# Kernel tuning notes

Hardware: AMD Instinct MI355X
Metric: run time of the kernel (lower is better)

Reference implementation:

```python
import jax, jax.numpy as jnp
import numpy as np

N = 50000          # nodes
E = 800000         # edges (before self-loops)
F_IN = 256         # feature_dim
HEADS = 3
OUT = 128          # per-head channels
HO = HEADS * OUT   # 384
NUM_GRAPHS = 64
NUM_CLASSES = 2
SLOPE = 0.2        # PyG GATConv default negative_slope


def setup_inputs() -> dict:
    key = jax.random.key(0)
    ks = jax.random.split(key, 8)
    x = jax.random.normal(ks[0], (N, F_IN), dtype=jnp.float32)
    edge_index = jax.random.randint(ks[1], (2, E), 0, N)
    batch = jnp.sort(jax.random.randint(ks[2], (N,), 0, NUM_GRAPHS))
    # GATConv params (glorot-ish scales)
    W = jax.random.normal(ks[3], (F_IN, HO), dtype=jnp.float32) * (1.0 / np.sqrt(F_IN))
    att_src = jax.random.normal(ks[4], (HEADS, OUT), dtype=jnp.float32) * 0.1
    att_dst = jax.random.normal(ks[5], (HEADS, OUT), dtype=jnp.float32) * 0.1
    bias = jnp.zeros((HO,), dtype=jnp.float32)
    fc_w = jax.random.normal(ks[6], (HO, NUM_CLASSES), dtype=jnp.float32) * 0.05
    fc_b = jnp.zeros((NUM_CLASSES,), dtype=jnp.float32)
    return {"x": x, "edge_index": edge_index, "batch": batch, "W": W,
            "att_src": att_src, "att_dst": att_dst, "bias": bias,
            "fc_w": fc_w, "fc_b": fc_b}


def reference(x, edge_index, batch, W, att_src, att_dst, bias, fc_w, fc_b):
    n = x.shape[0]
    h = (x @ W).reshape(n, HEADS, OUT)                      # [N, H, C]
    # add self-loops (PyG default add_self_loops=True)
    loops = jnp.arange(n)
    src = jnp.concatenate([edge_index[0], loops])           # [E+N]
    dst = jnp.concatenate([edge_index[1], loops])
    # per-node attention logits
    a_src = jnp.einsum('nhc,hc->nh', h, att_src)            # [N, H]
    a_dst = jnp.einsum('nhc,hc->nh', h, att_dst)
    e = jax.nn.leaky_relu(a_src[src] + a_dst[dst], SLOPE)   # [E+N, H]
    # segment softmax over incoming edges of each dst node
    emax = jax.ops.segment_max(e, dst, num_segments=n)
    ex = jnp.exp(e - emax[dst])
    denom = jax.ops.segment_sum(ex, dst, num_segments=n)
    alpha = ex / (denom[dst] + 1e-16)                       # [E+N, H]
    # weighted scatter-add aggregation
    msg = h[src] * alpha[:, :, None]                        # [E+N, H, C]
    out = jax.ops.segment_sum(msg, dst, num_segments=n)     # [N, H, C]
    out = jax.nn.relu(out.reshape(n, HO) + bias)            # [N, 384]
    # global mean pool per graph
    counts = jax.ops.segment_sum(jnp.ones((n,), out.dtype), batch,
                                 num_segments=NUM_GRAPHS)
    pooled = jax.ops.segment_sum(out, batch, num_segments=NUM_GRAPHS)
    pooled = pooled / jnp.maximum(counts, 1.0)[:, None]     # [G, 384]
    return pooled @ fc_w + fc_b                             # [G, num_classes]
```

## Files before the change

kernel.cpp:

```cpp
#include <hip/hip_runtime.h>
#include <hip/hip_bf16.h>
#include <math.h>

#define HEADS 3
#define HO 384
#define NGRAPH 64
#define F_IN 256
#define SLOPE 0.2f

typedef __attribute__((ext_vector_type(8))) short bf8;
typedef __attribute__((ext_vector_type(4))) float f4;
typedef __attribute__((ext_vector_type(2))) unsigned u2v;
typedef __attribute__((ext_vector_type(4))) unsigned u4v;

__device__ __forceinline__ unsigned short bfr(float f) {
    unsigned u = __float_as_uint(f);
    u += 0x7fffu + ((u >> 16) & 1u);
    return (unsigned short)(u >> 16);
}
__device__ __forceinline__ float bflo(unsigned u) { return __uint_as_float(u << 16); }
__device__ __forceinline__ float bfhi(unsigned u) { return __uint_as_float(u & 0xffff0000u); }
__device__ __forceinline__ float lrelu(float v) { return (v > 0.f) ? v : SLOPE * v; }

__device__ __forceinline__ void mix2(float& a0, float& a1, unsigned h2, float wm) {
    asm("v_fma_mix_f32 %0, %2, %3, %0 op_sel:[0,0,0] op_sel_hi:[1,0,0]\n\t"
        "v_fma_mix_f32 %1, %2, %3, %1 op_sel:[1,0,0] op_sel_hi:[1,0,0]"
        : "+v"(a0), "+v"(a1)
        : "v"(h2), "v"(wm));
}
__device__ __forceinline__ void dec8_mix(float* acc, float wm, unsigned ux, unsigned uy,
                                         unsigned c64) {
    unsigned p0 = __builtin_amdgcn_perm(ux, c64, 0x00050004u);
    unsigned p1 = __builtin_amdgcn_perm(ux, c64, 0x00070006u);
    unsigned p2 = __builtin_amdgcn_perm(uy, c64, 0x00050004u);
    unsigned p3 = __builtin_amdgcn_perm(uy, c64, 0x00070006u);
    mix2(acc[0], acc[1], p0, wm);
    mix2(acc[2], acc[3], p1, wm);
    mix2(acc[4], acc[5], p2, wm);
    mix2(acc[6], acc[7], p3, wm);
}

__global__ __launch_bounds__(256) void misc_k(const int* __restrict__ ei,
                                              const float* __restrict__ W,
                                              const int* __restrict__ batch,
                                              const float* __restrict__ X,
                                              int* __restrict__ count,
                                              int* __restrict__ rank,
                                              short* __restrict__ WbT,
                                              short* __restrict__ Xb,
                                              int* __restrict__ gstart,
                                              int NBc, int E, int N) {
    int b = blockIdx.x;
    if (b < NBc) {
        int e = b * 256 + threadIdx.x;
        int ET = E + N;
        if (e >= ET) return;
        int d = (e < E) ? ei[E + e] : (e - E);
        rank[e] = atomicAdd(&count[d], 1);
    } else if (b < NBc + 384) {
        int n = b - NBc;
        int k = threadIdx.x;
        WbT[n * 256 + k] = (short)bfr(W[(size_t)k * HO + n]);
    } else if (b == NBc + 384) {
        int g = threadIdx.x;
        if (g > NGRAPH) return;
        int lo = 0, hi = N;
        while (lo < hi) { int mid = (lo + hi) >> 1; if (batch[mid] < g) lo = mid + 1; else hi = mid; }
        gstart[g] = lo;
    } else {
        size_t base = (size_t)(b - (NBc + 385)) * 2048 + threadIdx.x * 8;
        if (base + 8 <= (size_t)N * F_IN) {
            float4 q0 = *(const float4*)(X + base);
            float4 q1 = *(const float4*)(X + base + 4);
            bf8 pk;
            pk[0] = (short)bfr(q0.x); pk[1] = (short)bfr(q0.y);
            pk[2] = (short)bfr(q0.z); pk[3] = (short)bfr(q0.w);
            pk[4] = (short)bfr(q1.x); pk[5] = (short)bfr(q1.y);
            pk[6] = (short)bfr(q1.z); pk[7] = (short)bfr(q1.w);
            *(bf8*)(Xb + base) = pk;
        }
    }
}

__global__ __launch_bounds__(256, 2) void gemm_att(const short* __restrict__ Xb,
                                                   const short* __restrict__ WbT,
                                                   const float* __restrict__ att_src,
                                                   const float* __restrict__ att_dst,
                                                   unsigned char* __restrict__ hc,
                                                   float* __restrict__ ni,
                                                   float* __restrict__ aDstO, int N) {
    __shared__ float lsS[64][8];
    __shared__ float lsD[64][8];
    __shared__ float lsM[64][8];
    __shared__ float sclS[64][4];
    int t = threadIdx.x;
    int w = t >> 6, lane = t & 63;
    int quad = lane >> 4, l15 = lane & 15;
    int rbase = blockIdx.x * 64;

    f4 acc[4][6] = {};
    const short* ap[4];
#pragma unroll
    for (int at = 0; at < 4; at++) {
        int r = rbase + at * 16 + l15;
        r = (r < N) ? r : (N - 1);
        ap[at] = Xb + (size_t)r * F_IN + quad * 8;
    }
    const short* bp = WbT + (size_t)(w * 96 + l15) * F_IN + quad * 8;

#pragma unroll
    for (int k0 = 0; k0 < F_IN; k0 += 32) {
        bf8 ar[4], br[6];
#pragma unroll
        for (int at = 0; at < 4; at++)
            ar[at] = *(const bf8*)(ap[at] + k0);
#pragma unroll
        for (int nt = 0; nt < 6; nt++)
            br[nt] = *(const bf8*)(bp + nt * 16 * F_IN + k0);
#pragma unroll
        for (int at = 0; at < 4; at++)
#pragma unroll
            for (int nt = 0; nt < 6; nt++)
                acc[at][nt] = __builtin_amdgcn_mfma_f32_16x16x32_bf16(ar[at], br[nt], acc[at][nt], 0, 0, 0);
    }

    const int splits[4] = {6, 2, 4, 0};
    int split = splits[w];
    float asv[6], adv[6];
#pragma unroll
    for (int nt = 0; nt < 6; nt++) {
        int c = w * 96 + nt * 16 + l15;
        asv[nt] = att_src[c];
        adv[nt] = att_dst[c];
    }
#pragma unroll
    for (int at = 0; at < 4; at++) {
#pragma unroll
        for (int r = 0; r < 4; r++) {
            float paS = 0.f, pbS = 0.f, paD = 0.f, pbD = 0.f;
#pragma unroll
            for (int nt = 0; nt < 6; nt++) {
                float v = acc[at][nt][r];
                if (nt < split) { paS += v * asv[nt]; paD += v * adv[nt]; }
                else            { pbS += v * asv[nt]; pbD += v * adv[nt]; }
            }
#pragma unroll
            for (int off = 1; off < 16; off <<= 1) {
                paS += __shfl_xor(paS, off); pbS += __shfl_xor(pbS, off);
                paD += __shfl_xor(paD, off); pbD += __shfl_xor(pbD, off);
            }
            if (l15 == 0) {
                int row = at * 16 + quad * 4 + r;
                lsS[row][w * 2 + 0] = paS; lsS[row][w * 2 + 1] = pbS;
                lsD[row][w * 2 + 0] = paD; lsD[row][w * 2 + 1] = pbD;
            }
        }
    }
#pragma unroll
    for (int at = 0; at < 4; at++) {
#pragma unroll
        for (int r = 0; r < 4; r++) {
            float pa = 0.f, pb = 0.f;
#pragma unroll
            for (int nt = 0; nt < 6; nt++) {
                float v = fabsf(acc[at][nt][r]);
                if (nt < split) pa = fmaxf(pa, v); else pb = fmaxf(pb, v);
            }
#pragma unroll
            for (int off = 1; off < 16; off <<= 1) {
                pa = fmaxf(pa, __shfl_xor(pa, off));
                pb = fmaxf(pb, __shfl_xor(pb, off));
            }
            if (l15 == 0) {
                int row = at * 16 + quad * 4 + r;
                lsM[row][w * 2 + 0] = pa; lsM[row][w * 2 + 1] = pb;
            }
        }
    }
    __syncthreads();
    if (t < 64) {
        float s0 = fmaxf(lsM[t][0], lsM[t][2]);
        float s1 = fmaxf(lsM[t][3], lsM[t][4]);
        float s2 = fmaxf(lsM[t][5], lsM[t][7]);
        sclS[t][0] = (s0 > 0.f) ? 127.f / s0 : 0.f;
        sclS[t][1] = (s1 > 0.f) ? 127.f / s1 : 0.f;
        sclS[t][2] = (s2 > 0.f) ? 127.f / s2 : 0.f;
        int node = rbase + t;
        if (node < N) {
            aDstO[node * 3 + 0] = lsD[t][0] + lsD[t][2];
            aDstO[node * 3 + 1] = lsD[t][3] + lsD[t][4];
            aDstO[node * 3 + 2] = lsD[t][5] + lsD[t][7];
            float4 nA, nB;
            nA.x = lsS[t][0] + lsS[t][2];
            nA.y = lsS[t][3] + lsS[t][4];
            nA.z = lsS[t][5] + lsS[t][7];
            nA.w = s0 / 127.f;
            nB.x = s1 / 127.f;
            nB.y = s2 / 127.f;
            nB.z = 0.f; nB.w = 0.f;
            *(float4*)(ni + (size_t)node * 8) = nA;
            *(float4*)(ni + (size_t)node * 8 + 4) = nB;
        }
    }
    __syncthreads();
#pragma unroll
    for (int at = 0; at < 4; at++) {
#pragma unroll
        for (int nt = 0; nt < 6; nt++) {
            int hd = (w * 96 + nt * 16) >> 7;
#pragma unroll
            for (int r = 0; r < 4; r++) {
                int row = at * 16 + quad * 4 + r;
                int node = rbase + row;
                float rq = sclS[row][hd];
                int qi = (int)rintf(acc[at][nt][r] * rq) + 128;
                if (node < N) hc[(size_t)node * 384 + w * 96 + nt * 16 + l15] = (unsigned char)qi;
            }
        }
    }
}

__global__ __launch_bounds__(256) void scan_a(const int* __restrict__ count,
                                              int* __restrict__ offsets,
                                              int* __restrict__ bsums, int N) {
    __shared__ int tmp[256];
    int t = threadIdx.x;
    int i = blockIdx.x * 256 + t;
    int v = (i < N) ? count[i] : 0;
    tmp[t] = v;
    __syncthreads();
    for (int off = 1; off < 256; off <<= 1) {
        int x = (t >= off) ? tmp[t - off] : 0;
        __syncthreads();
        tmp[t] += x;
        __syncthreads();
    }
    if (i < N) offsets[i] = tmp[t] - v;
    if (t == 255) bsums[blockIdx.x] = tmp[255];
}

__global__ __launch_bounds__(256) void scan_b(int* __restrict__ bsums, int NB) {
    __shared__ int tmp[256];
    int t = threadIdx.x;
    int v = (t < NB) ? bsums[t] : 0;
    tmp[t] = v;
    __syncthreads();
    for (int off = 1; off < 256; off <<= 1) {
        int x = (t >= off) ? tmp[t - off] : 0;
        __syncthreads();
        tmp[t] += x;
        __syncthreads();
    }
    if (t < NB) bsums[t] = tmp[t] - v;
}

__global__ __launch_bounds__(256) void scan_c(int* __restrict__ offsets,
                                              const int* __restrict__ bsums, int N) {
    int i = blockIdx.x * 256 + threadIdx.x;
    if (i < N) offsets[i] += bsums[blockIdx.x];
}

__global__ __launch_bounds__(256) void scatter_k(const int* __restrict__ ei,
                                                 const int* __restrict__ rank,
                                                 const int* __restrict__ offsets,
                                                 int* __restrict__ csr_src, int E, int N) {
    int e = blockIdx.x * 256 + threadIdx.x;
    int ET = E + N;
    if (e >= ET) return;
    int s, d;
    if (e < E) { s = ei[e]; d = ei[E + e]; } else { s = e - E; d = s; }
    csr_src[offsets[d] + rank[e]] = s;
}

__global__ __launch_bounds__(256) void aggregate_k(const unsigned* __restrict__ hcw,
                                                   const int* __restrict__ csr_src,
                                                   const int* __restrict__ offsets,
                                                   const int* __restrict__ count,
                                                   const float* __restrict__ ni,
                                                   const float* __restrict__ a_dst,
                                                   const float* __restrict__ bias,
                                                   unsigned* __restrict__ outb, int N) {
    __shared__ float ws[4][3][68];
    __shared__ int   si[4][64];
    int wv = threadIdx.x >> 6;
    int wid = blockIdx.x * 4 + wv;
    int lane = threadIdx.x & 63;
    if (wid >= N) return;
    int start = offsets[wid], n = count[wid];
    float ad0 = a_dst[wid * 3 + 0], ad1 = a_dst[wid * 3 + 1], ad2 = a_dst[wid * 3 + 2];
    int hm = (lane < 48) ? (lane >> 4) : 0;
    int off = (lane < 48) ? 2 * lane : 0;
    float acc[8] = {0.f, 0.f, 0.f, 0.f, 0.f, 0.f, 0.f, 0.f};
    float wsum = 0.f;
    float i0, i1, i2;
    const unsigned c64 = 0x64646464u;

    if (n <= 64) {
        int sreg = 0;
        float l0 = -INFINITY, l1 = -INFINITY, l2 = -INFINITY;
        float s0v = 0.f, s1v = 0.f, s2v = 0.f;
        if (lane < n) {
            sreg = csr_src[start + lane];
            float4 A = *(const float4*)(ni + (size_t)sreg * 8);
            float4 B = *(const float4*)(ni + (size_t)sreg * 8 + 4);
            l0 = lrelu(A.x + ad0); l1 = lrelu(A.y + ad1); l2 = lrelu(A.z + ad2);
            s0v = A.w; s1v = B.x; s2v = B.y;
        }
        float m0 = l0, m1 = l1, m2 = l2;
#pragma unroll
        for (int o = 1; o < 64; o <<= 1) {
            m0 = fmaxf(m0, __shfl_xor(m0, o));
            m1 = fmaxf(m1, __shfl_xor(m1, o));
            m2 = fmaxf(m2, __shfl_xor(m2, o));
        }
        float e0 = (lane < n) ? expf(l0 - m0) : 0.f;
        float e1 = (lane < n) ? expf(l1 - m1) : 0.f;
        float e2 = (lane < n) ? expf(l2 - m2) : 0.f;
        float s0 = e0, s1 = e1, s2 = e2;
#pragma unroll
        for (int o = 1; o < 64; o <<= 1) {
            s0 += __shfl_xor(s0, o);
            s1 += __shfl_xor(s1, o);
            s2 += __shfl_xor(s2, o);
        }
        i0 = 1.f / (s0 + 1e-16f); i1 = 1.f / (s1 + 1e-16f); i2 = 1.f / (s2 + 1e-16f);
        ws[wv][0][lane] = e0 * s0v;
        ws[wv][1][lane] = e1 * s1v;
        ws[wv][2][lane] = e2 * s2v;
        si[wv][lane] = sreg;
        __builtin_amdgcn_wave_barrier();

        for (int j = 0; j < n; j += 8) {
            int4 ia = *(const int4*)&si[wv][j];
            int4 ib = *(const int4*)&si[wv][j + 4];
            u2v u0 = *(const u2v*)(hcw + (size_t)ia.x * 96 + off);
            u2v u1 = *(const u2v*)(hcw + (size_t)ia.y * 96 + off);
            u2v u2 = *(const u2v*)(hcw + (size_t)ia.z * 96 + off);
            u2v u3 = *(const u2v*)(hcw + (size_t)ia.w * 96 + off);
            u2v u4 = *(const u2v*)(hcw + (size_t)ib.x * 96 + off);
            u2v u5 = *(const u2v*)(hcw + (size_t)ib.y * 96 + off);
            u2v u6 = *(const u2v*)(hcw + (size_t)ib.z * 96 + off);
            u2v u7 = *(const u2v*)(hcw + (size_t)ib.w * 96 + off);
            float4 wa = *(const float4*)&ws[wv][hm][j];
            float4 wb = *(const float4*)&ws[wv][hm][j + 4];
            wsum += (wa.x + wa.y + wa.z + wa.w) + (wb.x + wb.y + wb.z + wb.w);
            dec8_mix(acc, wa.x, u0.x, u0.y, c64);
            dec8_mix(acc, wa.y, u1.x, u1.y, c64);
            dec8_mix(acc, wa.z, u2.x, u2.y, c64);
            dec8_mix(acc, wa.w, u3.x, u3.y, c64);
            dec8_mix(acc, wb.x, u4.x, u4.y, c64);
            dec8_mix(acc, wb.y, u5.x, u5.y, c64);
            dec8_mix(acc, wb.z, u6.x, u6.y, c64);
            dec8_mix(acc, wb.w, u7.x, u7.y, c64);
        }
    } else {
        float m0 = -INFINITY, m1 = -INFINITY, m2 = -INFINITY;
        for (int j = lane; j < n; j += 64) {
            int s = csr_src[start + j];
            float4 A = *(const float4*)(ni + (size_t)s * 8);
            m0 = fmaxf(m0, lrelu(A.x + ad0));
            m1 = fmaxf(m1, lrelu(A.y + ad1));
            m2 = fmaxf(m2, lrelu(A.z + ad2));
        }
#pragma unroll
        for (int o = 1; o < 64; o <<= 1) {
            m0 = fmaxf(m0, __shfl_xor(m0, o));
            m1 = fmaxf(m1, __shfl_xor(m1, o));
            m2 = fmaxf(m2, __shfl_xor(m2, o));
        }
        float s0 = 0.f, s1 = 0.f, s2 = 0.f;
        for (int j = lane; j < n; j += 64) {
            int s = csr_src[start + j];
            float4 A = *(const float4*)(ni + (size_t)s * 8);
            s0 += expf(lrelu(A.x + ad0) - m0);
            s1 += expf(lrelu(A.y + ad1) - m1);
            s2 += expf(lrelu(A.z + ad2) - m2);
        }
#pragma unroll
        for (int o = 1; o < 64; o <<= 1) {
            s0 += __shfl_xor(s0, o);
            s1 += __shfl_xor(s1, o);
            s2 += __shfl_xor(s2, o);
        }
        i0 = 1.f / (s0 + 1e-16f); i1 = 1.f / (s1 + 1e-16f); i2 = 1.f / (s2 + 1e-16f);
        for (int j = 0; j < n; j++) {
            int s = csr_src[start + j];
            float4 A = *(const float4*)(ni + (size_t)s * 8);
            float4 B = *(const float4*)(ni + (size_t)s * 8 + 4);
            float w0 = expf(lrelu(A.x + ad0) - m0) * A.w;
            float w1 = expf(lrelu(A.y + ad1) - m1) * B.x;
            float w2 = expf(lrelu(A.z + ad2) - m2) * B.y;
            float wm = (hm == 0) ? w0 : ((hm == 1) ? w1 : w2);
            u2v u = *(const u2v*)(hcw + (size_t)s * 96 + off);
            wsum += wm;
            dec8_mix(acc, wm, u.x, u.y, c64);
        }
    }

    if (lane < 48) {
        float im = (hm == 0) ? i0 : ((hm == 1) ? i1 : i2);
        float corr = 1152.f * wsum;
        float4 b0 = *(const float4*)(bias + 8 * lane);
        float4 b1 = *(const float4*)(bias + 8 * lane + 4);
        float bb[8] = {b0.x, b0.y, b0.z, b0.w, b1.x, b1.y, b1.z, b1.w};
        u4v pk;
#pragma unroll
        for (int j = 0; j < 4; j++) {
            float x0 = (acc[2 * j] - corr) * im + bb[2 * j];
            float x1 = (acc[2 * j + 1] - corr) * im + bb[2 * j + 1];
            x0 = (x0 > 0.f) ? x0 : 0.f;
            x1 = (x1 > 0.f) ? x1 : 0.f;
            pk[j] = (unsigned)bfr(x0) | ((unsigned)bfr(x1) << 16);
        }
        *(u4v*)(outb + (size_t)wid * 192 + 4 * lane) = pk;
    }
}

__global__ __launch_bounds__(192) void pool_k(const unsigned* __restrict__ outb,
                                              const int* __restrict__ gstart,
                                              float* __restrict__ pooled) {
    int g = blockIdx.x;
    int chunk = blockIdx.y;
    int t = threadIdx.x;
    int lo = gstart[g], hi = gstart[g + 1];
    float al = 0.f, ah = 0.f;
    for (int r = lo + chunk; r < hi; r += 8) {
        unsigned u = outb[(size_t)r * 192 + t];
        al += bflo(u);
        ah += bfhi(u);
    }
    atomicAdd(&pooled[g * HO + 2 * t], al);
    atomicAdd(&pooled[g * HO + 2 * t + 1], ah);
}

__global__ __launch_bounds__(64) void fc_k(const float* __restrict__ pooled,
                                           const int* __restrict__ gstart,
                                           const float* __restrict__ fc_w,
                                           const float* __restrict__ fc_b,
                                           float* __restrict__ out) {
    int g = blockIdx.x;
    int lane = threadIdx.x;
    float a0 = 0.f, a1 = 0.f;
#pragma unroll
    for (int k = 0; k < 6; k++) {
        int c = lane + 64 * k;
        float pv = pooled[g * HO + c];
        a0 += pv * fc_w[c * 2 + 0];
        a1 += pv * fc_w[c * 2 + 1];
    }
#pragma unroll
    for (int off = 32; off > 0; off >>= 1) {
        a0 += __shfl_down(a0, off);
        a1 += __shfl_down(a1, off);
    }
    if (lane == 0) {
        float cnt = fmaxf((float)(gstart[g + 1] - gstart[g]), 1.0f);
        out[g * 2 + 0] = a0 / cnt + fc_b[0];
        out[g * 2 + 1] = a1 / cnt + fc_b[1];
    }
}

extern "C" void kernel_launch(void* const* d_in, const int* in_sizes, int n_in,
                              void* d_out, int out_size, void* d_ws, size_t ws_size,
                              hipStream_t stream) {
    const float* x       = (const float*)d_in[0];
    const int*   ei      = (const int*)d_in[1];
    const int*   batch   = (const int*)d_in[2];
    const float* W       = (const float*)d_in[3];
    const float* att_src = (const float*)d_in[4];
    const float* att_dst = (const float*)d_in[5];
    const float* bias    = (const float*)d_in[6];
    const float* fc_w    = (const float*)d_in[7];
    const float* fc_b    = (const float*)d_in[8];
    float* out = (float*)d_out;

    const int N = in_sizes[2];
    const int E = in_sizes[1] / 2;
    const int ET = E + N;

    char* p = (char*)d_ws;
    auto alloc = [&](size_t bytes) -> char* {
        char* r = p;
        p += (bytes + 255) & ~(size_t)255;
        return r;
    };
    short*         wbt    = (short*)alloc((size_t)HO * F_IN * 2);
    short*         xb     = (short*)alloc((size_t)N * F_IN * 2);
    unsigned char* hc     = (unsigned char*)alloc((size_t)N * 384);
    unsigned*      outb   = (unsigned*)alloc((size_t)N * 192 * 4);
    float*         ni     = (float*)alloc((size_t)N * 8 * 4);
    float*         a_dst  = (float*)alloc((size_t)N * 3 * 4);
    char*          zstart = p;
    int*           count  = (int*)alloc((size_t)N * 4);
    float*         pooled = (float*)alloc((size_t)NGRAPH * HO * 4);
    size_t         zbytes = (size_t)(p - zstart);
    int*           offsets = (int*)alloc((size_t)N * 4);
    int*           rank    = (int*)alloc((size_t)ET * 4);
    int*           bsums   = (int*)alloc(4096);
    int*           gstart  = (int*)alloc(1024);
    int*           csr_src = (int*)alloc((size_t)ET * 4);

    hipMemsetAsync(zstart, 0, zbytes, stream);

    int NBc = (ET + 255) / 256;
    int NXc = (int)(((size_t)N * F_IN + 2047) / 2048);
    misc_k<<<NBc + 384 + 1 + NXc, 256, 0, stream>>>(ei, W, batch, x, count, rank,
                                                    wbt, xb, gstart, NBc, E, N);
    gemm_att<<<(N + 63) / 64, 256, 0, stream>>>(xb, wbt, att_src, att_dst,
                                                hc, ni, a_dst, N);
    int NB = (N + 255) / 256;
    scan_a<<<NB, 256, 0, stream>>>(count, offsets, bsums, N);
    scan_b<<<1, 256, 0, stream>>>(bsums, NB);
    scan_c<<<NB, 256, 0, stream>>>(offsets, bsums, N);
    scatter_k<<<(ET + 255) / 256, 256, 0, stream>>>(ei, rank, offsets, csr_src, E, N);
    aggregate_k<<<(N + 3) / 4, 256, 0, stream>>>((const unsigned*)hc, csr_src, offsets,
                                                 count, ni, a_dst, bias, outb, N);
    dim3 pg(NGRAPH, 8);
    pool_k<<<pg, 192, 0, stream>>>(outb, gstart, pooled);
    fc_k<<<NGRAPH, 64, 0, stream>>>(pooled, gstart, fc_w, fc_b, out);

    (void)n_in; (void)out_size; (void)ws_size;
}
```

Baseline: 309.1 us.

## Fold attention vectors into weight matrix and compute logits via extra MFMA

Precomputes W·att_src and W·att_dst per head as a small bf16 matrix, so the attention logits come from an extra MFMA tile on one wave. This replaces the per-row dot products and shuffle reductions over the projected features in the epilogue. The GEMM tile is also halved to 32 rows with higher occupancy (launch bounds 4). Logits now come from the bf16-rounded folded weights rather than the fp32 accumulators, which slightly changes precision. The fourth wave also does extra MFMA work, adding imbalance across waves.

Result: no change. 308.3 us (-0.2%).

```diff
diff --git a/kernel.cpp b/kernel.cpp
--- a/kernel.cpp
+++ b/kernel.cpp
@@ -44,9 +44,12 @@
                                               const float* __restrict__ W,
                                               const int* __restrict__ batch,
                                               const float* __restrict__ X,
+                                              const float* __restrict__ att_src,
+                                              const float* __restrict__ att_dst,
                                               int* __restrict__ count,
                                               int* __restrict__ rank,
                                               short* __restrict__ WbT,
+                                              short* __restrict__ WaT,
                                               short* __restrict__ Xb,
                                               int* __restrict__ gstart,
                                               int NBc, int E, int N) {
@@ -67,8 +70,23 @@
         int lo = 0, hi = N;
         while (lo < hi) { int mid = (lo + hi) >> 1; if (batch[mid] < g) lo = mid + 1; else hi = mid; }
         gstart[g] = lo;
+    } else if (b == NBc + 385) {
+        int k = threadIdx.x;
+        float s[6] = {0.f, 0.f, 0.f, 0.f, 0.f, 0.f};
+        const float* wr = W + (size_t)k * HO;
+        for (int h = 0; h < 3; h++) {
+            float a0 = 0.f, a1 = 0.f;
+            for (int c = 0; c < 128; c++) {
+                float wv = wr[h * 128 + c];
+                a0 += wv * att_src[h * 128 + c];
+                a1 += wv * att_dst[h * 128 + c];
+            }
+            s[h] = a0; s[3 + h] = a1;
+        }
+        for (int c = 0; c < 6; c++)  WaT[c * 256 + k] = (short)bfr(s[c]);
+        for (int c = 6; c < 16; c++) WaT[c * 256 + k] = 0;
     } else {
-        size_t base = (size_t)(b - (NBc + 385)) * 2048 + threadIdx.x * 8;
+        size_t base = (size_t)(b - (NBc + 386)) * 2048 + threadIdx.x * 8;
         if (base + 8 <= (size_t)N * F_IN) {
             float4 q0 = *(const float4*)(X + base);
             float4 q1 = *(const float4*)(X + base + 4);
@@ -82,82 +100,57 @@
     }
 }
 
-__global__ __launch_bounds__(256, 2) void gemm_att(const short* __restrict__ Xb,
+__global__ __launch_bounds__(256, 4) void gemm_att(const short* __restrict__ Xb,
                                                    const short* __restrict__ WbT,
-                                                   const float* __restrict__ att_src,
-                                                   const float* __restrict__ att_dst,
+                                                   const short* __restrict__ WaT,
                                                    unsigned char* __restrict__ hc,
                                                    float* __restrict__ ni,
                                                    float* __restrict__ aDstO, int N) {
-    __shared__ float lsS[64][8];
-    __shared__ float lsD[64][8];
-    __shared__ float lsM[64][8];
-    __shared__ float sclS[64][4];
+    __shared__ float lsM[32][8];
+    __shared__ float lsA[32][6];
+    __shared__ float sclS[32][4];
     int t = threadIdx.x;
     int w = t >> 6, lane = t & 63;
     int quad = lane >> 4, l15 = lane & 15;
-    int rbase = blockIdx.x * 64;
-
-    f4 acc[4][6] = {};
-    const short* ap[4];
-#pragma unroll
-    for (int at = 0; at < 4; at++) {
+    int rbase = blockIdx.x * 32;
+
+    f4 acc[2][6] = {};
+    f4 acca[2] = {};
+    const short* ap[2];
+#pragma unroll
+    for (int at = 0; at < 2; at++) {
         int r = rbase + at * 16 + l15;
         r = (r < N) ? r : (N - 1);
         ap[at] = Xb + (size_t)r * F_IN + quad * 8;
     }
     const short* bp = WbT + (size_t)(w * 96 + l15) * F_IN + quad * 8;
+    const short* bpa = WaT + (size_t)l15 * F_IN + quad * 8;
 
 #pragma unroll
     for (int k0 = 0; k0 < F_IN; k0 += 32) {
-        bf8 ar[4], br[6];
-#pragma unroll
-        for (int at = 0; at < 4; at++)
+        bf8 ar[2], br[6];
+#pragma unroll
+        for (int at = 0; at < 2; at++)
             ar[at] = *(const bf8*)(ap[at] + k0);
 #pragma unroll
         for (int nt = 0; nt < 6; nt++)
             br[nt] = *(const bf8*)(bp + nt * 16 * F_IN + k0);
 #pragma unroll
-        for (int at = 0; at < 4; at++)
+        for (int at = 0; at < 2; at++)
 #pragma unroll
             for (int nt = 0; nt < 6; nt++)
                 acc[at][nt] = __builtin_amdgcn_mfma_f32_16x16x32_bf16(ar[at], br[nt], acc[at][nt], 0, 0, 0);
-    }
-
-    const int splits[4] = {6, 2, 4, 0};
+        if (w == 3) {
+            bf8 ba = *(const bf8*)(bpa + k0);
+            acca[0] = __builtin_amdgcn_mfma_f32_16x16x32_bf16(ar[0], ba, acca[0], 0, 0, 0);
+            acca[1] = __builtin_amdgcn_mfma_f32_16x16x32_bf16(ar[1], ba, acca[1], 0, 0, 0);
+        }
+    }
+
+    const int splits[4] = {6, 2, 4, 6};
     int split = splits[w];
-    float asv[6], adv[6];
-#pragma unroll
-    for (int nt = 0; nt < 6; nt++) {
-        int c = w * 96 + nt * 16 + l15;
-        asv[nt] = att_src[c];
-        adv[nt] = att_dst[c];
-    }
-#pragma unroll
-    for (int at = 0; at < 4; at++) {
-#pragma unroll
-        for (int r = 0; r < 4; r++) {
-            float paS = 0.f, pbS = 0.f, paD = 0.f, pbD = 0.f;
-#pragma unroll
-            for (int nt = 0; nt < 6; nt++) {
-                float v = acc[at][nt][r];
-                if (nt < split) { paS += v * asv[nt]; paD += v * adv[nt]; }
-                else            { pbS += v * asv[nt]; pbD += v * adv[nt]; }
-            }
-#pragma unroll
-            for (int off = 1; off < 16; off <<= 1) {
-                paS += __shfl_xor(paS, off); pbS += __shfl_xor(pbS, off);
-                paD += __shfl_xor(paD, off); pbD += __shfl_xor(pbD, off);
-            }
-            if (l15 == 0) {
-                int row = at * 16 + quad * 4 + r;
-                lsS[row][w * 2 + 0] = paS; lsS[row][w * 2 + 1] = pbS;
-                lsD[row][w * 2 + 0] = paD; lsD[row][w * 2 + 1] = pbD;
-            }
-        }
-    }
-#pragma unroll
-    for (int at = 0; at < 4; at++) {
+#pragma unroll
+    for (int at = 0; at < 2; at++) {
 #pragma unroll
         for (int r = 0; r < 4; r++) {
             float pa = 0.f, pb = 0.f;
@@ -177,23 +170,30 @@
             }
         }
     }
+    if (w == 3) {
+#pragma unroll
+        for (int at = 0; at < 2; at++)
+#pragma unroll
+            for (int r = 0; r < 4; r++)
+                if (l15 < 6) lsA[at * 16 + quad * 4 + r][l15] = acca[at][r];
+    }
     __syncthreads();
-    if (t < 64) {
+    if (t < 32) {
         float s0 = fmaxf(lsM[t][0], lsM[t][2]);
         float s1 = fmaxf(lsM[t][3], lsM[t][4]);
-        float s2 = fmaxf(lsM[t][5], lsM[t][7]);
+        float s2 = fmaxf(lsM[t][5], lsM[t][6]);
         sclS[t][0] = (s0 > 0.f) ? 127.f / s0 : 0.f;
         sclS[t][1] = (s1 > 0.f) ? 127.f / s1 : 0.f;
         sclS[t][2] = (s2 > 0.f) ? 127.f / s2 : 0.f;
         int node = rbase + t;
         if (node < N) {
-            aDstO[node * 3 + 0] = lsD[t][0] + lsD[t][2];
-            aDstO[node * 3 + 1] = lsD[t][3] + lsD[t][4];
-            aDstO[node * 3 + 2] = lsD[t][5] + lsD[t][7];
+            aDstO[node * 3 + 0] = lsA[t][3];
+            aDstO[node * 3 + 1] = lsA[t][4];
+            aDstO[node * 3 + 2] = lsA[t][5];
             float4 nA, nB;
-            nA.x = lsS[t][0] + lsS[t][2];
-            nA.y = lsS[t][3] + lsS[t][4];
-            nA.z = lsS[t][5] + lsS[t][7];
+            nA.x = lsA[t][0];
+            nA.y = lsA[t][1];
+            nA.z = lsA[t][2];
             nA.w = s0 / 127.f;
             nB.x = s1 / 127.f;
             nB.y = s2 / 127.f;
@@ -204,7 +204,7 @@
     }
     __syncthreads();
 #pragma unroll
-    for (int at = 0; at < 4; at++) {
+    for (int at = 0; at < 2; at++) {
 #pragma unroll
         for (int nt = 0; nt < 6; nt++) {
             int hd = (w * 96 + nt * 16) >> 7;
@@ -485,6 +485,7 @@
         return r;
     };
     short*         wbt    = (short*)alloc((size_t)HO * F_IN * 2);
+    short*         wat    = (short*)alloc((size_t)16 * F_IN * 2);
     short*         xb     = (short*)alloc((size_t)N * F_IN * 2);
     unsigned char* hc     = (unsigned char*)alloc((size_t)N * 384);
     unsigned*      outb   = (unsigned*)alloc((size_t)N * 192 * 4);
@@ -504,10 +505,10 @@
 
     int NBc = (ET + 255) / 256;
     int NXc = (int)(((size_t)N * F_IN + 2047) / 2048);
-    misc_k<<<NBc + 384 + 1 + NXc, 256, 0, stream>>>(ei, W, batch, x, count, rank,
-                                                    wbt, xb, gstart, NBc, E, N);
-    gemm_att<<<(N + 63) / 64, 256, 0, stream>>>(xb, wbt, att_src, att_dst,
-                                                hc, ni, a_dst, N);
+    misc_k<<<NBc + 386 + NXc, 256, 0, stream>>>(ei, W, batch, x, att_src, att_dst,
+                                                count, rank, wbt, wat, xb, gstart,
+                                                NBc, E, N);
+    gemm_att<<<(N + 31) / 32, 256, 0, stream>>>(xb, wbt, wat, hc, ni, a_dst, N);
     int NB = (N + 255) / 256;
     scan_a<<<NB, 256, 0, stream>>>(count, offsets, bsums, N);
     scan_b<<<1, 256, 0, stream>>>(bsums, NB);
```
